# Kernel tuning notes

Measured on AMD Instinct MI355X. Metric: run time of the kernel, lower is better.

The kernel has to match this reference:

```python
import jax, jax.numpy as jnp
import numpy as np
from jax import lax

HEADS = 8
DIM_HEAD = 64
INNER = HEADS * DIM_HEAD  # 512
LOG_SCALE_MAX = float(np.log(100.0))  # clamp for clamp_exp (SwinV2-style max temperature 1/0.01)
EPS_NORM = 1e-12  # F.normalize eps
EPS_LN = 1e-5


def setup_inputs() -> dict:
    key = jax.random.key(0)
    ks = jax.random.split(key, 6)
    b, c, h, w = 2, 256, 48, 48
    x = jax.random.normal(ks[0], (b, c, h, w), jnp.float32)
    w_in = jax.random.normal(ks[1], (3 * INNER, c), jnp.float32) * (c ** -0.5)
    b_in = jnp.zeros((3 * INNER,), jnp.float32)
    # learnable log-scale, init log(d_head ** -0.5), per head
    softmax_scale = jnp.full((HEADS, 1, 1), float(np.log(DIM_HEAD ** -0.5)), jnp.float32)
    w_dw = jax.random.normal(ks[2], (INNER, 1, 3, 3), jnp.float32) * (1.0 / 3.0)
    w_pw = jax.random.normal(ks[3], (2 * c, INNER), jnp.float32) * (INNER ** -0.5)
    gamma = jnp.full((2 * c,), 1e-3, jnp.float32)  # norm init_weight=0.001
    beta = jnp.zeros((2 * c,), jnp.float32)
    return {"x": x, "w_in": w_in, "b_in": b_in, "softmax_scale": softmax_scale,
            "w_dw": w_dw, "w_pw": w_pw, "gamma": gamma, "beta": beta}


def _l2norm(t):
    n = jnp.sqrt(jnp.sum(t * t, axis=-1, keepdims=True))
    return t / jnp.maximum(n, EPS_NORM)


def reference(x, w_in, b_in, softmax_scale, w_dw, w_pw, gamma, beta):
    b, c, h, w = x.shape
    s = h * w
    # proj_in: 1x1 conv then 'b (h c) x y -> b h x y c'
    y = jnp.einsum('bchw,oc->bohw', x, w_in) + b_in[None, :, None, None]
    y = y.reshape(b, HEADS, 3 * DIM_HEAD, h, w).transpose(0, 1, 3, 4, 2)  # b H x y (3*dh)
    y = y.reshape(b, HEADS, s, 3 * DIM_HEAD)
    q, k, v = jnp.split(y, 3, axis=-1)  # each [b, H, s, dh]
    # scaled cosine attention
    qn, kn = _l2norm(q), _l2norm(k)
    scale = jnp.exp(jnp.minimum(softmax_scale, LOG_SCALE_MAX))  # clamp_exp, [H,1,1]
    sim = jnp.einsum('bhid,bhjd->bhij', qn, kn) * scale[None]
    attn = jax.nn.softmax(sim, axis=-1)
    out = jnp.einsum('bhij,bhjd->bhid', attn, v)  # [b,H,s,dh]
    # unsplit heads -> 'b (h w) c' -> 'b c h w'
    update = out.transpose(0, 2, 1, 3).reshape(b, s, INNER)
    update = update.transpose(0, 2, 1).reshape(b, INNER, h, w)
    # proj_out: depthwise 3x3 (no bias) + pointwise 1x1 (no bias)
    dw = lax.conv_general_dilated(update, w_dw, (1, 1), 'SAME',
                                  feature_group_count=INNER,
                                  dimension_numbers=('NCHW', 'OIHW', 'NCHW'))
    pw = jnp.einsum('bchw,oc->bohw', dw, w_pw)  # [b, 2c, h, w]
    # channelwise layernorm with small init weight (norm_scales_and_shifts)
    mu = jnp.mean(pw, axis=1, keepdims=True)
    var = jnp.var(pw, axis=1, keepdims=True)
    normed = (pw - mu) * lax.rsqrt(var + EPS_LN)
    normed = normed * gamma[None, :, None, None] + beta[None, :, None, None]
    scales, shifts = jnp.split(normed, 2, axis=1)  # each [b, c, h, w]
    return shifts + x * scales
```

## Files before the change

kernel.cpp:

```cpp
#include <hip/hip_runtime.h>

#define B_ 2
#define C_ 256
#define S_ 2304
#define DH_ 64
#define O3_ 1536
#define INNER_ 512
#define LOGSMAX 4.605170185988092f
#define LOG2E 1.4426950408889634f

typedef __attribute__((ext_vector_type(8))) short short8;
typedef __attribute__((ext_vector_type(4))) float f32x4;
typedef __attribute__((ext_vector_type(16))) float f32x16;
typedef __attribute__((ext_vector_type(4))) unsigned short us4;
typedef __attribute__((ext_vector_type(4))) unsigned u32x4;
typedef __bf16 bf16x8 __attribute__((ext_vector_type(8)));

__device__ __forceinline__ unsigned short f2bf(float f) {
  unsigned u = __builtin_bit_cast(unsigned, f);
  u += 0x7FFFu + ((u >> 16) & 1u);
  return (unsigned short)(u >> 16);
}
__device__ __forceinline__ float bf2f(unsigned short h) {
  return __builtin_bit_cast(float, (unsigned)h << 16);
}
__device__ __forceinline__ bf16x8 as_bf(short8 v) {
  return __builtin_bit_cast(bf16x8, v);
}
__device__ __forceinline__ float fexp2(float x) {
#if __has_builtin(__builtin_amdgcn_exp2f)
  return __builtin_amdgcn_exp2f(x);
#else
  return __expf(x * 0.6931471805599453f);
#endif
}
__device__ __forceinline__ float frcp(float x) {
#if __has_builtin(__builtin_amdgcn_rcpf)
  return __builtin_amdgcn_rcpf(x);
#else
  return 1.f / x;
#endif
}
__device__ __forceinline__ unsigned pack_hi16(unsigned b, unsigned a) {
  return __builtin_amdgcn_perm(b, a, 0x07060302u);
}
__device__ __forceinline__ unsigned pk2(float a, float b) {
  unsigned ua = __builtin_bit_cast(unsigned, a) + 0x8000u;
  unsigned ub = __builtin_bit_cast(unsigned, b) + 0x8000u;
  return pack_hi16(ub, ua);
}

__global__ __launch_bounds__(256) void k_prep(const float* __restrict__ x,
                                              const float* __restrict__ w_in,
                                              const float* __restrict__ w_pw,
                                              unsigned short* __restrict__ xT,
                                              unsigned short* __restrict__ w_inb,
                                              unsigned short* __restrict__ w_pwb) {
  __shared__ float tile[64][65];
  int blk = blockIdx.x;
  int t = threadIdx.x;
  if (blk < 288) {
    int p0 = (blk % 36) * 64, c0 = ((blk / 36) % 4) * 64, b = blk / 144;
    const float* xb = x + (size_t)b * C_ * S_;
#pragma unroll
    for (int i = 0; i < 16; i++) {
      int c = i * 4 + (t >> 6);
      int p = t & 63;
      tile[c][p] = xb[(size_t)(c0 + c) * S_ + p0 + p];
    }
    __syncthreads();
    unsigned short* xTb = xT + (size_t)b * S_ * C_;
#pragma unroll
    for (int i = 0; i < 16; i++) {
      int p = i * 4 + (t >> 6);
      int c = t & 63;
      xTb[(size_t)(p0 + p) * C_ + c0 + c] = f2bf(tile[c][p]);
    }
  } else if (blk < 288 + 1536) {
    int i = (blk - 288) * 256 + t;
    w_inb[i] = f2bf(w_in[i]);
  } else {
    int i = (blk - 1824) * 256 + t;
    w_pwb[i] = f2bf(w_pw[i]);
  }
}

__global__ __launch_bounds__(256) void k_gemm_qkv(const unsigned short* __restrict__ A,
                                                  const unsigned short* __restrict__ BT,
                                                  const float* __restrict__ b_in,
                                                  const float* __restrict__ ss,
                                                  unsigned char* __restrict__ qn,
                                                  unsigned char* __restrict__ kn,
                                                  unsigned short* __restrict__ vT) {
  __shared__ __align__(16) unsigned short smem[64 * 72 + 128 * 72];
  unsigned short (*As)[72] = (unsigned short(*)[72])smem;
  unsigned short (*Bs)[72] = (unsigned short(*)[72])(smem + 64 * 72);
  int t = threadIdx.x;
  int lane = t & 63, wv = t >> 6;
  int quad = lane >> 4, r15 = lane & 15;
  int by = blockIdx.y;
  int m0 = by * 64, n0 = blockIdx.x * 128;
  int b = blockIdx.z;
  const unsigned short* BTb = BT + (size_t)b * S_ * C_;

  f32x4 acc[4][2] = {};

  int srA = t >> 2, scA = (t & 3) * 16;
  int srB = t >> 1, scB = (t & 1) * 32;
  const unsigned short* ag = A + (size_t)(m0 + srA) * C_ + scA;
  const unsigned short* bg = BTb + (size_t)(n0 + srB) * C_ + scB;

  for (int k0 = 0; k0 < C_; k0 += 64) {
    short8 a0 = *(const short8*)(ag + k0);
    short8 a1 = *(const short8*)(ag + k0 + 8);
    short8 b0 = *(const short8*)(bg + k0);
    short8 b1 = *(const short8*)(bg + k0 + 8);
    short8 b2 = *(const short8*)(bg + k0 + 16);
    short8 b3 = *(const short8*)(bg + k0 + 24);
    __syncthreads();
    *(short8*)&As[srA][scA] = a0;
    *(short8*)&As[srA][scA + 8] = a1;
    *(short8*)&Bs[srB][scB] = b0;
    *(short8*)&Bs[srB][scB + 8] = b1;
    *(short8*)&Bs[srB][scB + 16] = b2;
    *(short8*)&Bs[srB][scB + 24] = b3;
    __syncthreads();
#pragma unroll
    for (int ks = 0; ks < 2; ks++) {
      short8 af[4], bfr[2];
#pragma unroll
      for (int i = 0; i < 4; i++) af[i] = *(const short8*)&As[i * 16 + r15][ks * 32 + quad * 8];
#pragma unroll
      for (int j = 0; j < 2; j++) bfr[j] = *(const short8*)&Bs[wv * 32 + j * 16 + r15][ks * 32 + quad * 8];
#pragma unroll
      for (int i = 0; i < 4; i++)
#pragma unroll
        for (int j = 0; j < 2; j++)
          acc[i][j] = __builtin_amdgcn_mfma_f32_16x16x32_bf16(as_bf(af[i]), as_bf(bfr[j]), acc[i][j], 0, 0, 0);
    }
  }

  int h = by / 3, seg = by - h * 3;
  int bh = b * 8 + h;
  f32x4 bi[4];
#pragma unroll
  for (int i = 0; i < 4; i++) bi[i] = *(const f32x4*)&b_in[m0 + i * 16 + quad * 4];
  float bv[4][2][4];
  float ssq0 = 0.f, ssq1 = 0.f;
#pragma unroll
  for (int i = 0; i < 4; i++)
#pragma unroll
    for (int rr = 0; rr < 4; rr++) {
      float v0 = acc[i][0][rr] + bi[i][rr];
      float v1 = acc[i][1][rr] + bi[i][rr];
      bv[i][0][rr] = v0;
      bv[i][1][rr] = v1;
      ssq0 += v0 * v0;
      ssq1 += v1 * v1;
    }
  if (seg < 2) {
    float sc = (seg == 0) ? __expf(fminf(ss[h], LOGSMAX)) * LOG2E : 1.f;
    ssq0 += __shfl_xor(ssq0, 16);
    ssq0 += __shfl_xor(ssq0, 32);
    ssq1 += __shfl_xor(ssq1, 16);
    ssq1 += __shfl_xor(ssq1, 32);
    float inv0 = sc / fmaxf(sqrtf(ssq0), 1e-12f);
    float inv1 = sc / fmaxf(sqrtf(ssq1), 1e-12f);
    unsigned char* dst = (seg == 0 ? qn : kn) + (size_t)bh * S_ * DH_;
#pragma unroll
    for (int i = 0; i < 4; i++)
#pragma unroll
      for (int j = 0; j < 2; j++) {
        float iv = j ? inv1 : inv0;
        int pk = __builtin_amdgcn_cvt_pk_fp8_f32(bv[i][j][0] * iv, bv[i][j][1] * iv, 0, false);
        pk = __builtin_amdgcn_cvt_pk_fp8_f32(bv[i][j][2] * iv, bv[i][j][3] * iv, pk, true);
        int p = n0 + wv * 32 + j * 16 + r15;
        *(int*)&dst[(size_t)p * DH_ + i * 16 + quad * 4] = pk;
      }
  } else {
    __syncthreads();
    unsigned short* vt = smem;
#pragma unroll
    for (int i = 0; i < 4; i++)
#pragma unroll
      for (int j = 0; j < 2; j++) {
        int pcol = wv * 32 + j * 16 + r15;
#pragma unroll
        for (int rr = 0; rr < 4; rr++) {
          int d = i * 16 + quad * 4 + rr;
          vt[d * 132 + pcol] = f2bf(bv[i][j][rr]);
        }
      }
    __syncthreads();
    unsigned short* dst = vT + (size_t)bh * DH_ * S_;
    int dr = t >> 2, pc = (t & 3) * 32;
#pragma unroll
    for (int s2 = 0; s2 < 4; s2++) {
      short8 v8 = *(const short8*)&vt[dr * 132 + pc + s2 * 8];
      *(short8*)&dst[(size_t)dr * S_ + n0 + pc + s2 * 8] = v8;
    }
  }
}

__global__ __launch_bounds__(128) void k_gemm2(const unsigned short* __restrict__ A,
                                               const unsigned short* __restrict__ BT,
                                               unsigned short* __restrict__ outp,
                                               int M, int N, int K) {
  __shared__ __align__(16) unsigned short As[64][72];
  __shared__ __align__(16) unsigned short Bs[64][72];
  int t = threadIdx.x;
  int lane = t & 63, wv = t >> 6;
  int quad = lane >> 4, r15 = lane & 15;
  int m0 = blockIdx.y * 64, n0 = blockIdx.x * 64;
  int b = blockIdx.z;
  const unsigned short* BTb = BT + (size_t)b * N * K;

  f32x4 acc[4][2] = {};

  int sr = t >> 1, sc = (t & 1) * 32;
  const unsigned short* ag = A + (size_t)(m0 + sr) * K + sc;
  const unsigned short* bg = BTb + (size_t)(n0 + sr) * K + sc;

  for (int k0 = 0; k0 < K; k0 += 64) {
    short8 a0 = *(const short8*)(ag + k0);
    short8 a1 = *(const short8*)(ag + k0 + 8);
    short8 a2 = *(const short8*)(ag + k0 + 16);
    short8 a3 = *(const short8*)(ag + k0 + 24);
    short8 b0 = *(const short8*)(bg + k0);
    short8 b1 = *(const short8*)(bg + k0 + 8);
    short8 b2 = *(const short8*)(bg + k0 + 16);
    short8 b3 = *(const short8*)(bg + k0 + 24);
    __syncthreads();
    *(short8*)&As[sr][sc] = a0;
    *(short8*)&As[sr][sc + 8] = a1;
    *(short8*)&As[sr][sc + 16] = a2;
    *(short8*)&As[sr][sc + 24] = a3;
    *(short8*)&Bs[sr][sc] = b0;
    *(short8*)&Bs[sr][sc + 8] = b1;
    *(short8*)&Bs[sr][sc + 16] = b2;
    *(short8*)&Bs[sr][sc + 24] = b3;
    __syncthreads();
#pragma unroll
    for (int ks = 0; ks < 2; ks++) {
      short8 af[4], bfr[2];
#pragma unroll
      for (int i = 0; i < 4; i++) af[i] = *(const short8*)&As[i * 16 + r15][ks * 32 + quad * 8];
#pragma unroll
      for (int j = 0; j < 2; j++) bfr[j] = *(const short8*)&Bs[wv * 32 + j * 16 + r15][ks * 32 + quad * 8];
#pragma unroll
      for (int i = 0; i < 4; i++)
#pragma unroll
        for (int j = 0; j < 2; j++)
          acc[i][j] = __builtin_amdgcn_mfma_f32_16x16x32_bf16(as_bf(af[i]), as_bf(bfr[j]), acc[i][j], 0, 0, 0);
    }
  }
  unsigned short* Cb = outp + (size_t)b * M * N;
#pragma unroll
  for (int i = 0; i < 4; i++)
#pragma unroll
    for (int j = 0; j < 2; j++)
#pragma unroll
      for (int rr = 0; rr < 4; rr++) {
        int row = m0 + i * 16 + quad * 4 + rr;
        int col = n0 + wv * 32 + j * 16 + r15;
        Cb[(size_t)row * N + col] = f2bf(acc[i][j][rr]);
      }
}

__global__ __launch_bounds__(256) void k_attn(const unsigned char* __restrict__ qn,
                                              const unsigned char* __restrict__ kn,
                                              const unsigned short* __restrict__ vT,
                                              unsigned short* __restrict__ attnp,
                                              float* __restrict__ lp) {
  __shared__ __align__(16) unsigned char Ks[64][72];
  __shared__ __align__(16) unsigned short Vs[64][72];
  int t = threadIdx.x;
  int w = t >> 6;
  int lane = t & 63;
  int l31 = lane & 31, hi = lane >> 5;
  int bh = blockIdx.x;
  int q0 = blockIdx.y * 128 + w * 32;
  int split = blockIdx.z;
  int ktbase = split * 9;
  const unsigned char* qb = qn + (size_t)bh * S_ * DH_;
  const unsigned char* kb = kn + (size_t)bh * S_ * DH_;
  const unsigned short* vb = vT + (size_t)bh * DH_ * S_;

  const unsigned char* qrow = qb + (size_t)(q0 + l31) * DH_ + hi * 8;
  long qf[4];
#pragma unroll
  for (int ks = 0; ks < 4; ks++) qf[ks] = *(const long*)(qrow + ks * 16);

  const f32x16 z16 = {};
  f32x16 O0 = z16, O1 = z16;
  float l_part = 0.f;

  int srow = t >> 2;
  int scolK = (t & 3) * 16;
  int scolV = (t & 3) * 16;
  const unsigned char* kg = kb + ((size_t)(ktbase * 64) + srow) * DH_ + scolK;
  const unsigned short* vg = vb + (size_t)srow * S_ + ktbase * 64 + scolV;

  uint4 kr = *(const uint4*)kg;
  short8 vr0 = *(const short8*)vg;
  short8 vr1 = *(const short8*)(vg + 8);

  for (int i = 0; i < 9; i++) {
    __syncthreads();
    *(uint4*)&Ks[srow][scolK] = kr;
    *(short8*)&Vs[srow][scolV] = vr0;
    *(short8*)&Vs[srow][scolV + 8] = vr1;
    __syncthreads();
    if (i < 8) {
      kr = *(const uint4*)(kg + (size_t)(i + 1) * 64 * DH_);
      vr0 = *(const short8*)(vg + (i + 1) * 64);
      vr1 = *(const short8*)(vg + (i + 1) * 64 + 8);
    }
    f32x16 sc0, sc1;
    {
      long a0 = *(const long*)&Ks[l31][hi * 8];
      long a1 = *(const long*)&Ks[32 + l31][hi * 8];
      sc0 = __builtin_amdgcn_mfma_f32_32x32x16_fp8_fp8(a0, qf[0], z16, 0, 0, 0);
      sc1 = __builtin_amdgcn_mfma_f32_32x32x16_fp8_fp8(a1, qf[0], z16, 0, 0, 0);
    }
#pragma unroll
    for (int ks = 1; ks < 4; ks++) {
      long a0 = *(const long*)&Ks[l31][ks * 16 + hi * 8];
      long a1 = *(const long*)&Ks[32 + l31][ks * 16 + hi * 8];
      sc0 = __builtin_amdgcn_mfma_f32_32x32x16_fp8_fp8(a0, qf[ks], sc0, 0, 0, 0);
      sc1 = __builtin_amdgcn_mfma_f32_32x32x16_fp8_fp8(a1, qf[ks], sc1, 0, 0, 0);
    }
#pragma unroll
    for (int mt = 0; mt < 2; mt++) {
      const f32x16& s = mt ? sc1 : sc0;
      unsigned pk[8];
      float lsum = 0.f;
#pragma unroll
      for (int g2 = 0; g2 < 4; g2++) {
        float e0 = fexp2(s[g2 * 4 + 0]);
        float e1 = fexp2(s[g2 * 4 + 1]);
        float e2 = fexp2(s[g2 * 4 + 2]);
        float e3 = fexp2(s[g2 * 4 + 3]);
        lsum += (e0 + e1) + (e2 + e3);
        pk[2 * g2] = pk2(e0, e1);
        pk[2 * g2 + 1] = pk2(e2, e3);
      }
      l_part += lsum;
#pragma unroll
      for (int half = 0; half < 2; half++) {
        int gb = half * 4;
        unsigned ya = hi ? pk[gb + 0] : pk[gb + 2];
        unsigned yb = hi ? pk[gb + 1] : pk[gb + 3];
        unsigned ra = __shfl_xor(ya, 32);
        unsigned rb = __shfl_xor(yb, 32);
        u32x4 fd;
        fd[0] = hi ? ra : pk[gb + 0];
        fd[1] = hi ? rb : pk[gb + 1];
        fd[2] = hi ? pk[gb + 2] : ra;
        fd[3] = hi ? pk[gb + 3] : rb;
        short8 pb = __builtin_bit_cast(short8, fd);
        int ks = mt * 2 + half;
        short8 va0 = *(const short8*)&Vs[l31][ks * 16 + hi * 8];
        short8 va1 = *(const short8*)&Vs[32 + l31][ks * 16 + hi * 8];
        O0 = __builtin_amdgcn_mfma_f32_32x32x16_bf16(as_bf(va0), as_bf(pb), O0, 0, 0, 0);
        O1 = __builtin_amdgcn_mfma_f32_32x32x16_bf16(as_bf(va1), as_bf(pb), O1, 0, 0, 0);
      }
    }
  }
  float l = l_part + __shfl_xor(l_part, 32);
  if (hi == 0) lp[((size_t)(split * 16 + bh)) * S_ + q0 + l31] = l;
  unsigned short* orow = attnp + (((size_t)(split * 16 + bh)) * S_ + q0 + l31) * DH_;
#pragma unroll
  for (int mt = 0; mt < 2; mt++) {
    const f32x16& O = mt ? O1 : O0;
#pragma unroll
    for (int g = 0; g < 4; g++) {
      us4 o4 = {f2bf(O[g * 4 + 0]), f2bf(O[g * 4 + 1]), f2bf(O[g * 4 + 2]), f2bf(O[g * 4 + 3])};
      *(us4*)&orow[mt * 32 + g * 8 + hi * 4] = o4;
    }
  }
}

__global__ __launch_bounds__(256) void k_dwconv(const unsigned short* __restrict__ attnp,
                                                const float* __restrict__ lp,
                                                const float* __restrict__ w_dw,
                                                unsigned short* __restrict__ dwb) {
  __shared__ float sc[3][6][64];
  int t = threadIdx.x;
  int d = t & 63;
  int wv = t >> 6;
  int bh = blockIdx.x;
  int b = bh >> 3, h = bh & 7;
  int p0 = blockIdx.y * 4;
  int x0 = p0 % 48, y0 = p0 / 48;
  const unsigned short* a0 = attnp + (size_t)bh * S_ * DH_ + d;
  const unsigned short* a1 = attnp + ((size_t)(16 + bh)) * S_ * DH_ + d;
  const unsigned short* a2 = attnp + ((size_t)(32 + bh)) * S_ * DH_ + d;
  const unsigned short* a3 = attnp + ((size_t)(48 + bh)) * S_ * DH_ + d;
  const float* l0 = lp + (size_t)bh * S_;
  const float* l1 = lp + (size_t)(16 + bh) * S_;
  const float* l2 = lp + (size_t)(32 + bh) * S_;
  const float* l3 = lp + (size_t)(48 + bh) * S_;
  for (int i = wv; i < 18; i += 4) {
    int ry = i / 6, cx = i - ry * 6;
    int y2 = y0 + ry - 1, x2 = x0 + cx - 1;
    float val = 0.f;
    if (y2 >= 0 && y2 < 48 && x2 >= 0 && x2 < 48) {
      int p2 = y2 * 48 + x2;
      float rl = frcp(l0[p2] + l1[p2] + l2[p2] + l3[p2]);
      val = (bf2f(a0[(size_t)p2 * DH_]) + bf2f(a1[(size_t)p2 * DH_]) +
             bf2f(a2[(size_t)p2 * DH_]) + bf2f(a3[(size_t)p2 * DH_])) * rl;
    }
    sc[ry][cx][d] = val;
  }
  __syncthreads();
  int ch = h * 64 + d;
  float w[9];
#pragma unroll
  for (int i = 0; i < 9; i++) w[i] = w_dw[ch * 9 + i];
  float acc = 0.f;
#pragma unroll
  for (int dy = 0; dy < 3; dy++)
#pragma unroll
    for (int dx = 0; dx < 3; dx++)
      acc += sc[dy][wv + dx][d] * w[dy * 3 + dx];
  dwb[((size_t)b * S_ + p0 + wv) * INNER_ + ch] = f2bf(acc);
}

__global__ __launch_bounds__(256) void k_ln_final(const unsigned short* __restrict__ pw,
                                                  const float* __restrict__ gamma,
                                                  const float* __restrict__ beta,
                                                  const float* __restrict__ x,
                                                  float* __restrict__ out) {
  __shared__ float s_s0[32][8], s_s1[32][8], s_q0[32][8], s_q1[32][8];
  int t = threadIdx.x;
  int pl = t & 7, g = t >> 3;
  int b = blockIdx.y;
  int p = blockIdx.x * 16 + pl * 2;
  const unsigned short* pwb = pw + (size_t)b * INNER_ * S_ + p;
  float s0 = 0.f, s1 = 0.f, q0 = 0.f, q1 = 0.f;
#pragma unroll
  for (int j = 0; j < 16; j++) {
    unsigned u = *(const unsigned*)&pwb[(size_t)(g * 16 + j) * S_];
    float vx = bf2f((unsigned short)(u & 0xffffu));
    float vy = bf2f((unsigned short)(u >> 16));
    s0 += vx; s1 += vy;
    q0 += vx * vx; q1 += vy * vy;
  }
  s_s0[g][pl] = s0; s_s1[g][pl] = s1;
  s_q0[g][pl] = q0; s_q1[g][pl] = q1;
  __syncthreads();
  float t0 = 0.f, t1 = 0.f, u0 = 0.f, u1 = 0.f;
#pragma unroll
  for (int i = 0; i < 32; i++) {
    t0 += s_s0[i][pl]; t1 += s_s1[i][pl];
    u0 += s_q0[i][pl]; u1 += s_q1[i][pl];
  }
  float mu0 = t0 * (1.f / 512.f), mu1 = t1 * (1.f / 512.f);
  float rs0 = rsqrtf(u0 * (1.f / 512.f) - mu0 * mu0 + 1e-5f);
  float rs1 = rsqrtf(u1 * (1.f / 512.f) - mu1 * mu1 + 1e-5f);
  const float* xb = x + (size_t)b * C_ * S_ + p;
  float* ob = out + (size_t)b * C_ * S_ + p;
#pragma unroll
  for (int j = 0; j < 8; j++) {
    int cc = g * 8 + j;
    float ga = gamma[cc], be = beta[cc];
    float gs = gamma[cc + 256], bs = beta[cc + 256];
    unsigned pu = *(const unsigned*)&pwb[(size_t)cc * S_];
    unsigned su = *(const unsigned*)&pwb[(size_t)(cc + 256) * S_];
    float2 xv = *(const float2*)&xb[(size_t)cc * S_];
    float pv0 = bf2f((unsigned short)(pu & 0xffffu));
    float pv1 = bf2f((unsigned short)(pu >> 16));
    float sv0 = bf2f((unsigned short)(su & 0xffffu));
    float sv1 = bf2f((unsigned short)(su >> 16));
    float sc0 = (pv0 - mu0) * rs0 * ga + be;
    float sc1 = (pv1 - mu1) * rs1 * ga + be;
    float sh0 = (sv0 - mu0) * rs0 * gs + bs;
    float sh1 = (sv1 - mu1) * rs1 * gs + bs;
    float2 o;
    o.x = sh0 + xv.x * sc0;
    o.y = sh1 + xv.y * sc1;
    *(float2*)&ob[(size_t)cc * S_] = o;
  }
}

extern "C" void kernel_launch(void* const* d_in, const int* in_sizes, int n_in,
                              void* d_out, int out_size, void* d_ws, size_t ws_size,
                              hipStream_t stream) {
  const float* x = (const float*)d_in[0];
  const float* w_in = (const float*)d_in[1];
  const float* b_in = (const float*)d_in[2];
  const float* ss = (const float*)d_in[3];
  const float* w_dw = (const float*)d_in[4];
  const float* w_pw = (const float*)d_in[5];
  const float* gamma = (const float*)d_in[6];
  const float* beta = (const float*)d_in[7];
  float* out = (float*)d_out;
  char* ws = (char*)d_ws;

  unsigned short* xT = (unsigned short*)(ws + 0);
  unsigned short* w_inb = (unsigned short*)(ws + 2359296);
  unsigned short* w_pwb = (unsigned short*)(ws + 3145728);
  unsigned char* qn = (unsigned char*)(ws + 3670016);
  unsigned char* kn = (unsigned char*)(ws + 6029312);
  unsigned short* vT = (unsigned short*)(ws + 8388608);
  unsigned short* dwb = (unsigned short*)(ws + 13107200);
  float* lp = (float*)(ws + 17825792);
  unsigned short* attnp = (unsigned short*)(ws + 18415616);
  unsigned short* pw = (unsigned short*)(ws + 37289984);

  k_prep<<<2848, 256, 0, stream>>>(x, w_in, w_pw, xT, w_inb, w_pwb);
  k_gemm_qkv<<<dim3(18, 24, 2), 256, 0, stream>>>(w_inb, xT, b_in, ss, qn, kn, vT);
  k_attn<<<dim3(16, 18, 4), 256, 0, stream>>>(qn, kn, vT, attnp, lp);
  k_dwconv<<<dim3(16, 576), 256, 0, stream>>>(attnp, lp, w_dw, dwb);
  k_gemm2<<<dim3(36, 8, 2), 128, 0, stream>>>(w_pwb, dwb, pw, INNER_, S_, INNER_);
  k_ln_final<<<dim3(144, 2), 256, 0, stream>>>(pw, gamma, beta, x, out);
}
```

Baseline: 153.0 us.

## Double-buffer K/V tiles in attention and vectorize weight conversion

The attention kernel now keeps two LDS buffers for K and V. The next tile is written into the alternate buffer while the current one is consumed, which cuts the two barriers per iteration down to one and prefetches two tiles ahead from global memory. The prep kernel converts the weights four floats at a time with vector loads and stores, which shrinks its grid. The cost is doubled LDS use per block, which may lower occupancy, and more live registers.

```diff
diff --git a/kernel.cpp b/kernel.cpp
--- a/kernel.cpp
+++ b/kernel.cpp
@@ -76,12 +76,16 @@
       int c = t & 63;
       xTb[(size_t)(p0 + p) * C_ + c0 + c] = f2bf(tile[c][p]);
     }
-  } else if (blk < 288 + 1536) {
-    int i = (blk - 288) * 256 + t;
-    w_inb[i] = f2bf(w_in[i]);
+  } else if (blk < 288 + 384) {
+    int i = ((blk - 288) * 256 + t) * 4;
+    f32x4 f = *(const f32x4*)&w_in[i];
+    us4 o = {f2bf(f[0]), f2bf(f[1]), f2bf(f[2]), f2bf(f[3])};
+    *(us4*)&w_inb[i] = o;
   } else {
-    int i = (blk - 1824) * 256 + t;
-    w_pwb[i] = f2bf(w_pw[i]);
+    int i = ((blk - 672) * 256 + t) * 4;
+    f32x4 f = *(const f32x4*)&w_pw[i];
+    us4 o = {f2bf(f[0]), f2bf(f[1]), f2bf(f[2]), f2bf(f[3])};
+    *(us4*)&w_pwb[i] = o;
   }
 }
 
@@ -272,8 +276,8 @@
                                               const unsigned short* __restrict__ vT,
                                               unsigned short* __restrict__ attnp,
                                               float* __restrict__ lp) {
-  __shared__ __align__(16) unsigned char Ks[64][72];
-  __shared__ __align__(16) unsigned short Vs[64][72];
+  __shared__ __align__(16) unsigned char Ks[2][64][72];
+  __shared__ __align__(16) unsigned short Vs[2][64][72];
   int t = threadIdx.x;
   int w = t >> 6;
   int lane = t & 63;
@@ -301,32 +305,42 @@
   const unsigned char* kg = kb + ((size_t)(ktbase * 64) + srow) * DH_ + scolK;
   const unsigned short* vg = vb + (size_t)srow * S_ + ktbase * 64 + scolV;
 
-  uint4 kr = *(const uint4*)kg;
-  short8 vr0 = *(const short8*)vg;
-  short8 vr1 = *(const short8*)(vg + 8);
+  {
+    uint4 k0 = *(const uint4*)kg;
+    short8 v0a = *(const short8*)vg;
+    short8 v0b = *(const short8*)(vg + 8);
+    *(uint4*)&Ks[0][srow][scolK] = k0;
+    *(short8*)&Vs[0][srow][scolV] = v0a;
+    *(short8*)&Vs[0][srow][scolV + 8] = v0b;
+  }
+  uint4 kr = *(const uint4*)(kg + (size_t)64 * DH_);
+  short8 vr0 = *(const short8*)(vg + 64);
+  short8 vr1 = *(const short8*)(vg + 64 + 8);
+  __syncthreads();
 
   for (int i = 0; i < 9; i++) {
-    __syncthreads();
-    *(uint4*)&Ks[srow][scolK] = kr;
-    *(short8*)&Vs[srow][scolV] = vr0;
-    *(short8*)&Vs[srow][scolV + 8] = vr1;
-    __syncthreads();
+    int cur = i & 1;
     if (i < 8) {
-      kr = *(const uint4*)(kg + (size_t)(i + 1) * 64 * DH_);
-      vr0 = *(const short8*)(vg + (i + 1) * 64);
-      vr1 = *(const short8*)(vg + (i + 1) * 64 + 8);
+      *(uint4*)&Ks[cur ^ 1][srow][scolK] = kr;
+      *(short8*)&Vs[cur ^ 1][srow][scolV] = vr0;
+      *(short8*)&Vs[cur ^ 1][srow][scolV + 8] = vr1;
+      if (i < 7) {
+        kr = *(const uint4*)(kg + (size_t)(i + 2) * 64 * DH_);
+        vr0 = *(const short8*)(vg + (i + 2) * 64);
+        vr1 = *(const short8*)(vg + (i + 2) * 64 + 8);
+      }
     }
     f32x16 sc0, sc1;
     {
-      long a0 = *(const long*)&Ks[l31][hi * 8];
-      long a1 = *(const long*)&Ks[32 + l31][hi * 8];
+      long a0 = *(const long*)&Ks[cur][l31][hi * 8];
+      long a1 = *(const long*)&Ks[cur][32 + l31][hi * 8];
       sc0 = __builtin_amdgcn_mfma_f32_32x32x16_fp8_fp8(a0, qf[0], z16, 0, 0, 0);
       sc1 = __builtin_amdgcn_mfma_f32_32x32x16_fp8_fp8(a1, qf[0], z16, 0, 0, 0);
     }
 #pragma unroll
     for (int ks = 1; ks < 4; ks++) {
-      long a0 = *(const long*)&Ks[l31][ks * 16 + hi * 8];
-      long a1 = *(const long*)&Ks[32 + l31][ks * 16 + hi * 8];
+      long a0 = *(const long*)&Ks[cur][l31][ks * 16 + hi * 8];
+      long a1 = *(const long*)&Ks[cur][32 + l31][ks * 16 + hi * 8];
       sc0 = __builtin_amdgcn_mfma_f32_32x32x16_fp8_fp8(a0, qf[ks], sc0, 0, 0, 0);
       sc1 = __builtin_amdgcn_mfma_f32_32x32x16_fp8_fp8(a1, qf[ks], sc1, 0, 0, 0);
     }
@@ -360,12 +374,13 @@
         fd[3] = hi ? pk[gb + 3] : rb;
         short8 pb = __builtin_bit_cast(short8, fd);
         int ks = mt * 2 + half;
-        short8 va0 = *(const short8*)&Vs[l31][ks * 16 + hi * 8];
-        short8 va1 = *(const short8*)&Vs[32 + l31][ks * 16 + hi * 8];
+        short8 va0 = *(const short8*)&Vs[cur][l31][ks * 16 + hi * 8];
+        short8 va1 = *(const short8*)&Vs[cur][32 + l31][ks * 16 + hi * 8];
         O0 = __builtin_amdgcn_mfma_f32_32x32x16_bf16(as_bf(va0), as_bf(pb), O0, 0, 0, 0);
         O1 = __builtin_amdgcn_mfma_f32_32x32x16_bf16(as_bf(va1), as_bf(pb), O1, 0, 0, 0);
       }
     }
+    __syncthreads();
   }
   float l = l_part + __shfl_xor(l_part, 32);
   if (hi == 0) lp[((size_t)(split * 16 + bh)) * S_ + q0 + l31] = l;
@@ -509,7 +524,7 @@
   unsigned short* attnp = (unsigned short*)(ws + 18415616);
   unsigned short* pw = (unsigned short*)(ws + 37289984);
 
-  k_prep<<<2848, 256, 0, stream>>>(x, w_in, w_pw, xT, w_inb, w_pwb);
+  k_prep<<<928, 256, 0, stream>>>(x, w_in, w_pw, xT, w_inb, w_pwb);
   k_gemm_qkv<<<dim3(18, 24, 2), 256, 0, stream>>>(w_inb, xT, b_in, ss, qn, kn, vT);
   k_attn<<<dim3(16, 18, 4), 256, 0, stream>>>(qn, kn, vT, attnp, lp);
   k_dwconv<<<dim3(16, 576), 256, 0, stream>>>(attnp, lp, w_dw, dwb);
```

New measurement: 151.3 us. Within noise of the previous version (-1.1%).
